# Kernel tuning notes

Measured on AMD Instinct MI355X. Metric: run time of the kernel, lower is better.

## Reference

```python
import jax, jax.numpy as jnp
import numpy as np

NEG = -1e30  # log-space -inf surrogate (safe for logaddexp in fp32)


def _ctc_mean_loss(y_true, y_pred):
    """tf.nn.ctc_loss with blank_index=-1, logit_length=T, label_length=#nonzero.

    y_true: [B, L] int labels, 0 = padding, packed at the front.
    y_pred: [B, T, C] logits. blank = C-1. Returns mean NLL over batch.
    """
    B, L = y_true.shape
    T, C = y_pred.shape[1], y_pred.shape[2]
    blank = C - 1
    S = 2 * L + 1  # extended label length (blanks interleaved)

    label_length = jnp.sum((y_true != 0).astype(jnp.int32), axis=1)  # [B]
    logp = jax.nn.log_softmax(y_pred, axis=-1)  # [B, T, C]

    # Extended sequence: blank, l1, blank, l2, ..., blank
    ext = jnp.full((B, S), blank, dtype=jnp.int32)
    ext = ext.at[:, 1::2].set(y_true.astype(jnp.int32))  # [B, S]

    # skip transition (s-2 -> s) allowed only at odd s>=3 when labels differ
    skip_ok = jnp.zeros((B, S), dtype=bool)
    skip_ok = skip_ok.at[:, 3::2].set(y_true[:, 1:] != y_true[:, :-1])

    # alpha_0
    alpha0 = jnp.full((B, S), NEG, dtype=logp.dtype)
    alpha0 = alpha0.at[:, 0].set(logp[:, 0, blank])
    alpha0 = alpha0.at[:, 1].set(
        jnp.take_along_axis(logp[:, 0, :], ext[:, 1:2], axis=1)[:, 0])

    def step(alpha, logp_t):  # alpha [B,S], logp_t [B,C]
        s1 = jnp.pad(alpha, ((0, 0), (1, 0)), constant_values=NEG)[:, :-1]
        s2 = jnp.pad(alpha, ((0, 0), (2, 0)), constant_values=NEG)[:, :-2]
        comb = jnp.logaddexp(jnp.logaddexp(alpha, s1),
                             jnp.where(skip_ok, s2, NEG))
        emit = jnp.take_along_axis(logp_t, ext, axis=1)  # [B,S]
        return comb + emit, None

    alphaT, _ = jax.lax.scan(step, alpha0, jnp.swapaxes(logp, 0, 1)[1:])

    # P(labels) = alpha_T[2l] + alpha_T[2l-1]  (last blank / last label)
    l = label_length
    idx = jnp.stack([2 * l, 2 * l - 1], axis=1)  # [B,2], l>=1 by construction
    fin = jnp.take_along_axis(alphaT, idx, axis=1)
    loss = -jnp.logaddexp(fin[:, 0], fin[:, 1])  # [B]
    return jnp.mean(loss)


def setup_inputs() -> dict:
    key = jax.random.key(0)
    k1, k2, k3 = jax.random.split(key, 3)
    B, T, L, C = 256, 512, 128, 128
    lengths = jax.random.randint(k1, (B,), L // 2, L + 1)  # labels per example
    vals = jax.random.randint(k2, (B, L), 1, C - 1)  # classes 1..C-2 (blank=C-1)
    mask = jnp.arange(L)[None, :] < lengths[:, None]
    y_true = jnp.where(mask, vals, 0).astype(jnp.int32)
    y_pred = jax.random.normal(k3, (B, T, C), dtype=jnp.float32)
    return {"y_true": y_true, "y_pred": y_pred}


def reference(y_true, y_pred):
    return _ctc_mean_loss(y_true, y_pred)
```

## Files before the change

kernel.cpp:

```cpp
#include <hip/hip_runtime.h>
#include <hip/hip_fp16.h>

#define LN2D 0.6931471805599453094172321

typedef float v2f __attribute__((ext_vector_type(2)));

__device__ __forceinline__ float shr1(float v, float fill) {
    return __int_as_float(__builtin_amdgcn_update_dpp(
        __float_as_int(fill), __float_as_int(v), 0x138 , 0xF, 0xF, false));
}
__device__ __forceinline__ float shl1(float v, float fill) {
    return __int_as_float(__builtin_amdgcn_update_dpp(
        __float_as_int(fill), __float_as_int(v), 0x130 , 0xF, 0xF, false));
}

__device__ __forceinline__ float wave_sum63(float x) {
    int t;
    t = __builtin_amdgcn_update_dpp(0, __float_as_int(x), 0x111, 0xF, 0xF, true);
    x += __int_as_float(t);
    t = __builtin_amdgcn_update_dpp(0, __float_as_int(x), 0x112, 0xF, 0xF, true);
    x += __int_as_float(t);
    t = __builtin_amdgcn_update_dpp(0, __float_as_int(x), 0x114, 0xF, 0xF, true);
    x += __int_as_float(t);
    t = __builtin_amdgcn_update_dpp(0, __float_as_int(x), 0x118, 0xF, 0xF, true);
    x += __int_as_float(t);
    t = __builtin_amdgcn_update_dpp(0, __float_as_int(x), 0x142, 0xA, 0xF, true);
    x += __int_as_float(t);
    t = __builtin_amdgcn_update_dpp(0, __float_as_int(x), 0x143, 0xC, 0xF, true);
    x += __int_as_float(t);
    return x;
}

__device__ __forceinline__ float wave_max63(float x) {
    int iv = __float_as_int(x); int t;
    t = __builtin_amdgcn_update_dpp(iv, iv, 0x111, 0xF, 0xF, false);
    x = fmaxf(x, __int_as_float(t)); iv = __float_as_int(x);
    t = __builtin_amdgcn_update_dpp(iv, iv, 0x112, 0xF, 0xF, false);
    x = fmaxf(x, __int_as_float(t)); iv = __float_as_int(x);
    t = __builtin_amdgcn_update_dpp(iv, iv, 0x114, 0xF, 0xF, false);
    x = fmaxf(x, __int_as_float(t)); iv = __float_as_int(x);
    t = __builtin_amdgcn_update_dpp(iv, iv, 0x118, 0xF, 0xF, false);
    x = fmaxf(x, __int_as_float(t)); iv = __float_as_int(x);
    t = __builtin_amdgcn_update_dpp(iv, iv, 0x142, 0xA, 0xF, false);
    x = fmaxf(x, __int_as_float(t)); iv = __float_as_int(x);
    t = __builtin_amdgcn_update_dpp(iv, iv, 0x143, 0xC, 0xF, false);
    x = fmaxf(x, __int_as_float(t));
    return x;
}

__device__ __forceinline__ float rdl63(float v) {
    return __int_as_float(__builtin_amdgcn_readlane(__float_as_int(v), 63));
}

#define VSTRIDE 260

__global__ __launch_bounds__(256) void ctc_half(const int* __restrict__ yt,
                                                const float* __restrict__ yp,
                                                float* __restrict__ V,
                                                int* __restrict__ E,
                                                float* __restrict__ accW) {
    constexpr int L = 128;
    const int bh   = blockIdx.x;
    const int b    = bh >> 1, h = bh & 1;
    const int w    = threadIdx.x >> 6;
    const int lane = threadIdx.x & 63;

    __shared__ int g[256][64];

    const int2 cc = *reinterpret_cast<const int2*>(yt + b * L + 2 * lane);
    const int c1 = cc.x, c3 = cc.y;
    const int sl1 = c1 >> 1, sh1v = (c1 & 1) << 4;
    const int sl3 = c3 >> 1, sh3v = (c3 & 1) << 4;

    float acc = 0.0f;
    const float* src = yp + ((size_t)b * 512 + h * 256 + w * 64) * 128 + lane * 2;
    v2f A8[8], B8[8];

#define ISSUE8(d_, p_)                                                         \
    asm volatile(                                                              \
        "global_load_dwordx2 %0, %8, off\n\t"                                  \
        "global_load_dwordx2 %1, %8, off offset:512\n\t"                       \
        "global_load_dwordx2 %2, %8, off offset:1024\n\t"                      \
        "global_load_dwordx2 %3, %8, off offset:1536\n\t"                      \
        "global_load_dwordx2 %4, %8, off offset:2048\n\t"                      \
        "global_load_dwordx2 %5, %8, off offset:2560\n\t"                      \
        "global_load_dwordx2 %6, %8, off offset:3072\n\t"                      \
        "global_load_dwordx2 %7, %8, off offset:3584"                          \
        : "=&v"(d_[0]), "=&v"(d_[1]), "=&v"(d_[2]), "=&v"(d_[3]),              \
          "=&v"(d_[4]), "=&v"(d_[5]), "=&v"(d_[6]), "=&v"(d_[7])               \
        : "v"(p_)                                                              \
        : "memory");

#define WAITN(n_)                                                              \
    {                                                                          \
        asm volatile("s_waitcnt vmcnt(" #n_ ")" ::: "memory");                 \
        __builtin_amdgcn_sched_barrier(0);                                     \
    }

#define PROC8(buf_, rb_)                                                       \
    {                                                                          \
        _Pragma("unroll")                                                      \
        for (int i = 0; i < 8; ++i) {                                          \
            const float vx = buf_[i].x, vy = buf_[i].y;                        \
            const float sall = rdl63(wave_sum63(__expf(vx) + __expf(vy)));     \
            const float xbv  = rdl63(vy);                \
            acc += __logf(sall) - xbv;                                         \
            const __half2 hh = __floats2half2_rn(vx, vy);                      \
            const int hb = __builtin_bit_cast(int, hh);                        \
            const int q1 = __shfl(hb, sl1, 64);                                \
            const int q3 = __shfl(hb, sl3, 64);                                \
            const float x1 = __half2float(__builtin_bit_cast(__half, (unsigned short)(q1 >> sh1v))); \
            const float x3 = __half2float(__builtin_bit_cast(__half, (unsigned short)(q3 >> sh3v))); \
            g[w * 64 + (rb_) + i][lane] =                                      \
                __builtin_bit_cast(int, __floats2half2_rn(x1 - xbv, x3 - xbv)); \
        }                                                                      \
    }

    ISSUE8(A8, src)
    ISSUE8(B8, src + 8 * 128)
    WAITN(8)  PROC8(A8, 0)   ISSUE8(A8, src + 16 * 128)
    WAITN(8)  PROC8(B8, 8)   ISSUE8(B8, src + 24 * 128)
    WAITN(8)  PROC8(A8, 16)  ISSUE8(A8, src + 32 * 128)
    WAITN(8)  PROC8(B8, 24)  ISSUE8(B8, src + 40 * 128)
    WAITN(8)  PROC8(A8, 32)  ISSUE8(A8, src + 48 * 128)
    WAITN(8)  PROC8(B8, 40)  ISSUE8(B8, src + 56 * 128)
    WAITN(8)  PROC8(A8, 48)
    WAITN(0)  PROC8(B8, 56)

    if (lane == 0) accW[bh * 4 + w] = acc;
    __syncthreads();

    if (w == 0) {
        const int cprev = __shfl_up(c3, 1, 64);
        const float sk1 = (lane > 0 && c1 != cprev) ? 1.0f : 0.0f;
        const float sk3 = (c3 != c1) ? 1.0f : 0.0f;
        const float skB3 = shl1(sk1, 0.0f);
        const int llen = __popcll(__ballot(c1 != 0)) + __popcll(__ballot(c3 != 0));

        float o0, o1, o2, o3, o4;
        int   Eacc = 0;

#define RENORM()                                                               \
    {                                                                          \
        float mr = fmaxf(fmaxf(fmaxf(o0, o1), fmaxf(o2, o3)), o4);             \
        const float mru = rdl63(wave_max63(mr));                               \
        const int ie = (__float_as_int(mru) >> 23) & 0xFF;                     \
        const float sc = __int_as_float((253 - ie) << 23);                     \
        o0 *= sc; o1 *= sc; o2 *= sc; o3 *= sc; o4 *= sc;                      \
        Eacc += ie - 126;                                                      \
    }

#define FSTEP(bits_, rn_)                                                      \
    {                                                                          \
        const float2 dd = __half22float2(__builtin_bit_cast(__half2, (bits_)));\
        const float e1 = __expf(dd.x);                                         \
        const float e3 = __expf(dd.y);                                         \
        const float pm = shr1(o3, 0.0f);                                       \
        const float n0 = o0 + pm;                                              \
        const float n1 = (o1 + o0 + sk1 * pm) * e1;                            \
        const float n2 = o2 + o1;                                              \
        const float n3 = (o3 + o2 + sk3 * o1) * e3;                            \
        o4 += o3;                                                              \
        o0 = n0; o1 = n1; o2 = n2; o3 = n3;                                    \
        if (rn_) RENORM();                                                     \
    }

#define BSTEP(bits_, rn_)                                                      \
    {                                                                          \
        const float2 dd = __half22float2(__builtin_bit_cast(__half2, (bits_)));\
        const float g1 = o1 * __expf(dd.x);                                    \
        const float g3 = o3 * __expf(dd.y);                                    \
        const float pm0 = shl1(o0, o4);          \
        const float pm1 = shl1(g1, 0.0f);        \
        const float n0 = o0 + g1;                                              \
        const float n1 = g1 + o2 + sk3 * g3;                                   \
        const float n2 = o2 + g3;                                              \
        const float n3 = g3 + pm0 + skB3 * pm1;                                \
        o0 = n0; o1 = n1; o2 = n2; o3 = n3;                                    \
        if (rn_) RENORM();                                                     \
    }

        if (h == 0) {
            {
                const float2 d0 = __half22float2(__builtin_bit_cast(__half2, g[0][lane]));
                o0 = (lane == 0) ? 1.0f : 0.0f;
                o1 = (lane == 0) ? __expf(d0.x) : 0.0f;
                o2 = 0.0f; o3 = 0.0f; o4 = 0.0f;
            }
            #pragma unroll
            for (int t = 1; t < 32; ++t) FSTEP(g[t][lane], false);
            for (int tb = 32; tb < 256; tb += 32) {
                #pragma unroll
                for (int j = 0; j < 32; ++j) FSTEP(g[tb + j][lane], (j == 0));
            }
        } else {
            const int sA = 2 * llen, sB = 2 * llen - 1;
            o0 = (4 * lane + 0 == sA) ? 1.0f : 0.0f;
            o1 = (4 * lane + 1 == sB) ? 1.0f : 0.0f;
            o2 = (4 * lane + 2 == sA) ? 1.0f : 0.0f;
            o3 = (4 * lane + 3 == sB) ? 1.0f : 0.0f;
            o4 = (llen == 128 && lane == 63) ? 1.0f : 0.0f;
            for (int sb = 0; sb < 256; sb += 32) {
                #pragma unroll
                for (int u = 1; u <= 32; ++u) BSTEP(g[256 - (sb + u)][lane], (u == 32));
            }
        }

        float* Vh = V + (size_t)bh * VSTRIDE;
        Vh[4 * lane + 0] = o0; Vh[4 * lane + 1] = o1;
        Vh[4 * lane + 2] = o2; Vh[4 * lane + 3] = o3;
        if (lane == 63) Vh[256] = o4;
        if (lane == 0)  E[bh] = Eacc;
#undef BSTEP
#undef FSTEP
#undef RENORM
    }
#undef PROC8
#undef WAITN
#undef ISSUE8
}

__global__ __launch_bounds__(64) void combine(const float* __restrict__ V,
                                              const int* __restrict__ E,
                                              const float* __restrict__ accW,
                                              float* __restrict__ loss) {
    const int b = blockIdx.x, lane = threadIdx.x;
    const float* Vf = V + (size_t)(2 * b) * VSTRIDE;
    const float* Vb = Vf + VSTRIDE;
    const float4 a = *reinterpret_cast<const float4*>(Vf + 4 * lane);
    const float4 c = *reinterpret_cast<const float4*>(Vb + 4 * lane);
    double p = (double)a.x * (double)c.x + (double)a.y * (double)c.y
             + (double)a.z * (double)c.z + (double)a.w * (double)c.w;
    if (lane == 63) p += (double)Vf[256] * (double)Vb[256];
    #pragma unroll
    for (int off = 32; off > 0; off >>= 1) p += __shfl_xor(p, off, 64);
    if (lane == 0) {
        float ls = 0.0f;
        #pragma unroll
        for (int j = 0; j < 8; ++j) ls += accW[8 * b + j];
        const double lg = log(p) + (double)(E[2 * b] + E[2 * b + 1]) * LN2D - (double)ls;
        loss[b] = -(float)lg;
    }
}

__global__ __launch_bounds__(256) void finalize(const float* __restrict__ loss,
                                                float* __restrict__ out) {
    __shared__ float red[256];
    const int tid = threadIdx.x;
    red[tid] = loss[tid];
    __syncthreads();
    for (int off = 128; off > 0; off >>= 1) {
        if (tid < off) red[tid] += red[tid + off];
        __syncthreads();
    }
    if (tid == 0) out[0] = red[0] * (1.0f / 256.0f);
}

extern "C" void kernel_launch(void* const* d_in, const int* in_sizes, int n_in,
                              void* d_out, int out_size, void* d_ws, size_t ws_size,
                              hipStream_t stream) {
    constexpr int B = 256;
    const int*   y_true = (const int*)d_in[0];
    const float* y_pred = (const float*)d_in[1];
    float* out = (float*)d_out;

    float* V    = (float*)d_ws;
    int*   E    = (int*)(V + 512 * VSTRIDE);
    float* accW = (float*)(E + 512);
    float* loss = accW + 2048;

    ctc_half<<<B * 2, 256, 0, stream>>>(y_true, y_pred, V, E, accW);
    combine<<<B, 64, 0, stream>>>(V, E, accW, loss);
    finalize<<<1, 256, 0, stream>>>(loss, out);
}
```

Baseline: 43.95 us.

## Store precomputed bf16 emission probabilities and prefetch LDS rows in recursion

```diff
diff --git a/kernel.cpp b/kernel.cpp
--- a/kernel.cpp
+++ b/kernel.cpp
@@ -50,6 +50,13 @@
 
 __device__ __forceinline__ float rdl63(float v) {
     return __int_as_float(__builtin_amdgcn_readlane(__float_as_int(v), 63));
+}
+
+__device__ __forceinline__ int pk_bf16(float a, float b) {
+    unsigned ua = __float_as_uint(a), ub = __float_as_uint(b);
+    ua = (ua + 0x7FFFu + ((ua >> 16) & 1u)) >> 16;
+    ub = (ub + 0x7FFFu + ((ub >> 16) & 1u)) & 0xFFFF0000u;
+    return (int)(ua | ub);
 }
 
 #define VSTRIDE 260
@@ -112,7 +119,7 @@
             const float x1 = __half2float(__builtin_bit_cast(__half, (unsigned short)(q1 >> sh1v))); \
             const float x3 = __half2float(__builtin_bit_cast(__half, (unsigned short)(q3 >> sh3v))); \
             g[w * 64 + (rb_) + i][lane] =                                      \
-                __builtin_bit_cast(int, __floats2half2_rn(x1 - xbv, x3 - xbv)); \
+                pk_bf16(__expf(x1 - xbv), __expf(x3 - xbv));                   \
         }                                                                      \
     }
 
@@ -139,6 +146,7 @@
 
         float o0, o1, o2, o3, o4;
         int   Eacc = 0;
+        int   er[8];
 
 #define RENORM()                                                               \
     {                                                                          \
@@ -152,9 +160,8 @@
 
 #define FSTEP(bits_, rn_)                                                      \
     {                                                                          \
-        const float2 dd = __half22float2(__builtin_bit_cast(__half2, (bits_)));\
-        const float e1 = __expf(dd.x);                                         \
-        const float e3 = __expf(dd.y);                                         \
+        const float e1 = __int_as_float((bits_) << 16);                        \
+        const float e3 = __int_as_float((bits_) & 0xFFFF0000);                 \
         const float pm = shr1(o3, 0.0f);                                       \
         const float n0 = o0 + pm;                                              \
         const float n1 = (o1 + o0 + sk1 * pm) * e1;                            \
@@ -167,9 +174,10 @@
 
 #define BSTEP(bits_, rn_)                                                      \
     {                                                                          \
-        const float2 dd = __half22float2(__builtin_bit_cast(__half2, (bits_)));\
-        const float g1 = o1 * __expf(dd.x);                                    \
-        const float g3 = o3 * __expf(dd.y);                                    \
+        const float e1 = __int_as_float((bits_) << 16);                        \
+        const float e3 = __int_as_float((bits_) & 0xFFFF0000);                 \
+        const float g1 = o1 * e1;                                              \
+        const float g3 = o3 * e3;                                              \
         const float pm0 = shl1(o0, o4);          \
         const float pm1 = shl1(g1, 0.0f);        \
         const float n0 = o0 + g1;                                              \
@@ -181,29 +189,47 @@
     }
 
         if (h == 0) {
+            #pragma unroll
+            for (int i = 0; i < 8; ++i) er[i] = g[i][lane];
             {
-                const float2 d0 = __half22float2(__builtin_bit_cast(__half2, g[0][lane]));
+                const float e10 = __int_as_float(er[0] << 16);
                 o0 = (lane == 0) ? 1.0f : 0.0f;
-                o1 = (lane == 0) ? __expf(d0.x) : 0.0f;
+                o1 = (lane == 0) ? e10 : 0.0f;
                 o2 = 0.0f; o3 = 0.0f; o4 = 0.0f;
             }
-            #pragma unroll
-            for (int t = 1; t < 32; ++t) FSTEP(g[t][lane], false);
-            for (int tb = 32; tb < 256; tb += 32) {
+            er[0] = g[8][lane];
+            #pragma unroll
+            for (int t = 1; t < 8; ++t) { FSTEP(er[t], false); er[t] = g[t + 8][lane]; }
+            #pragma unroll
+            for (int tb = 8; tb < 248; tb += 8) {
                 #pragma unroll
-                for (int j = 0; j < 32; ++j) FSTEP(g[tb + j][lane], (j == 0));
+                for (int j = 0; j < 8; ++j) {
+                    FSTEP(er[j], ((tb + j) & 31) == 0);
+                    er[j] = g[tb + j + 8][lane];
+                }
             }
+            #pragma unroll
+            for (int t = 248; t < 256; ++t) FSTEP(er[t & 7], false);
         } else {
+            #pragma unroll
+            for (int i = 0; i < 8; ++i) er[i] = g[255 - i][lane];
             const int sA = 2 * llen, sB = 2 * llen - 1;
             o0 = (4 * lane + 0 == sA) ? 1.0f : 0.0f;
             o1 = (4 * lane + 1 == sB) ? 1.0f : 0.0f;
             o2 = (4 * lane + 2 == sA) ? 1.0f : 0.0f;
             o3 = (4 * lane + 3 == sB) ? 1.0f : 0.0f;
             o4 = (llen == 128 && lane == 63) ? 1.0f : 0.0f;
-            for (int sb = 0; sb < 256; sb += 32) {
+            #pragma unroll
+            for (int kb = 0; kb < 248; kb += 8) {
                 #pragma unroll
-                for (int u = 1; u <= 32; ++u) BSTEP(g[256 - (sb + u)][lane], (u == 32));
+                for (int j = 0; j < 8; ++j) {
+                    const int r = 255 - (kb + j);
+                    BSTEP(er[j], (r & 31) == 0);
+                    er[j] = g[r - 8][lane];
+                }
             }
+            #pragma unroll
+            for (int k = 248; k < 256; ++k) BSTEP(er[k & 7], ((255 - k) & 31) == 0);
         }
 
         float* Vh = V + (size_t)bh * VSTRIDE;
```

Result: faster. 40.80 us (median of 2 runs) (-7.2%).

## Fuse forward/backward CTC halves into one block with interleaved recursions and fp8 emissions

Applied to the files above, without the earlier changes.

```diff
diff --git a/kernel.cpp b/kernel.cpp
--- a/kernel.cpp
+++ b/kernel.cpp
@@ -52,20 +52,30 @@
     return __int_as_float(__builtin_amdgcn_readlane(__float_as_int(v), 63));
 }
 
-#define VSTRIDE 260
-
-__global__ __launch_bounds__(256) void ctc_half(const int* __restrict__ yt,
-                                                const float* __restrict__ yp,
-                                                float* __restrict__ V,
-                                                int* __restrict__ E,
-                                                float* __restrict__ accW) {
+__device__ __forceinline__ unsigned short pk_fp8(float a, float b) {
+    const unsigned short ha = __builtin_bit_cast(unsigned short, __float2half_rn(a));
+    const unsigned short hb = __builtin_bit_cast(unsigned short, __float2half_rn(b));
+    const unsigned ua = ((unsigned)ha + 0x80u) >> 8;
+    const unsigned ub = (((unsigned)hb + 0x80u) >> 8) << 8;
+    return (unsigned short)(ua | ub);
+}
+__device__ __forceinline__ float dec_lo(unsigned short u) {
+    return __half2float(__builtin_bit_cast(__half, (unsigned short)((u & 0xFFu) << 8)));
+}
+__device__ __forceinline__ float dec_hi(unsigned short u) {
+    return __half2float(__builtin_bit_cast(__half, (unsigned short)(u & 0xFF00u)));
+}
+
+__global__ __launch_bounds__(512) void ctc_fused(const int* __restrict__ yt,
+                                                 const float* __restrict__ yp,
+                                                 float* __restrict__ part,
+                                                 float* __restrict__ accW) {
     constexpr int L = 128;
-    const int bh   = blockIdx.x;
-    const int b    = bh >> 1, h = bh & 1;
+    const int b    = blockIdx.x;
     const int w    = threadIdx.x >> 6;
     const int lane = threadIdx.x & 63;
 
-    __shared__ int g[256][64];
+    __shared__ unsigned short g[512][64];
 
     const int2 cc = *reinterpret_cast<const int2*>(yt + b * L + 2 * lane);
     const int c1 = cc.x, c3 = cc.y;
@@ -73,7 +83,7 @@
     const int sl3 = c3 >> 1, sh3v = (c3 & 1) << 4;
 
     float acc = 0.0f;
-    const float* src = yp + ((size_t)b * 512 + h * 256 + w * 64) * 128 + lane * 2;
+    const float* src = yp + ((size_t)b * 512 + w * 64) * 128 + lane * 2;
     v2f A8[8], B8[8];
 
 #define ISSUE8(d_, p_)                                                         \
@@ -111,8 +121,7 @@
             const int q3 = __shfl(hb, sl3, 64);                                \
             const float x1 = __half2float(__builtin_bit_cast(__half, (unsigned short)(q1 >> sh1v))); \
             const float x3 = __half2float(__builtin_bit_cast(__half, (unsigned short)(q3 >> sh3v))); \
-            g[w * 64 + (rb_) + i][lane] =                                      \
-                __builtin_bit_cast(int, __floats2half2_rn(x1 - xbv, x3 - xbv)); \
+            g[w * 64 + (rb_) + i][lane] = pk_fp8(__expf(x1 - xbv), __expf(x3 - xbv)); \
         }                                                                      \
     }
 
@@ -127,7 +136,7 @@
     WAITN(8)  PROC8(A8, 48)
     WAITN(0)  PROC8(B8, 56)
 
-    if (lane == 0) accW[bh * 4 + w] = acc;
+    if (lane == 0) accW[b * 8 + w] = acc;
     __syncthreads();
 
     if (w == 0) {
@@ -138,23 +147,24 @@
         const int llen = __popcll(__ballot(c1 != 0)) + __popcll(__ballot(c3 != 0));
 
         float o0, o1, o2, o3, o4;
-        int   Eacc = 0;
-
-#define RENORM()                                                               \
-    {                                                                          \
-        float mr = fmaxf(fmaxf(fmaxf(o0, o1), fmaxf(o2, o3)), o4);             \
+        float q0, q1, q2, q3, q4;
+        int   EF = 0, EB = 0;
+        unsigned short fr[8], br[8];
+
+#define RENORM5(a0_, a1_, a2_, a3_, a4_, Ec_)                                  \
+    {                                                                          \
+        float mr = fmaxf(fmaxf(fmaxf(a0_, a1_), fmaxf(a2_, a3_)), a4_);        \
         const float mru = rdl63(wave_max63(mr));                               \
         const int ie = (__float_as_int(mru) >> 23) & 0xFF;                     \
         const float sc = __int_as_float((253 - ie) << 23);                     \
-        o0 *= sc; o1 *= sc; o2 *= sc; o3 *= sc; o4 *= sc;                      \
-        Eacc += ie - 126;                                                      \
+        a0_ *= sc; a1_ *= sc; a2_ *= sc; a3_ *= sc; a4_ *= sc;                 \
+        Ec_ += ie - 126;                                                       \
     }
 
 #define FSTEP(bits_, rn_)                                                      \
     {                                                                          \
-        const float2 dd = __half22float2(__builtin_bit_cast(__half2, (bits_)));\
-        const float e1 = __expf(dd.x);                                         \
-        const float e3 = __expf(dd.y);                                         \
+        const float e1 = dec_lo(bits_);                                        \
+        const float e3 = dec_hi(bits_);                                        \
         const float pm = shr1(o3, 0.0f);                                       \
         const float n0 = o0 + pm;                                              \
         const float n1 = (o1 + o0 + sk1 * pm) * e1;                            \
@@ -162,92 +172,91 @@
         const float n3 = (o3 + o2 + sk3 * o1) * e3;                            \
         o4 += o3;                                                              \
         o0 = n0; o1 = n1; o2 = n2; o3 = n3;                                    \
-        if (rn_) RENORM();                                                     \
+        if (rn_) RENORM5(o0, o1, o2, o3, o4, EF);                              \
     }
 
 #define BSTEP(bits_, rn_)                                                      \
     {                                                                          \
-        const float2 dd = __half22float2(__builtin_bit_cast(__half2, (bits_)));\
-        const float g1 = o1 * __expf(dd.x);                                    \
-        const float g3 = o3 * __expf(dd.y);                                    \
-        const float pm0 = shl1(o0, o4);          \
+        const float e1 = dec_lo(bits_);                                        \
+        const float e3 = dec_hi(bits_);                                        \
+        const float g1 = q1 * e1;                                              \
+        const float g3 = q3 * e3;                                              \
+        const float pm0 = shl1(q0, q4);          \
         const float pm1 = shl1(g1, 0.0f);        \
-        const float n0 = o0 + g1;                                              \
-        const float n1 = g1 + o2 + sk3 * g3;                                   \
-        const float n2 = o2 + g3;                                              \
+        const float n0 = q0 + g1;                                              \
+        const float n1 = g1 + q2 + sk3 * g3;                                   \
+        const float n2 = q2 + g3;                                              \
         const float n3 = g3 + pm0 + skB3 * pm1;                                \
-        o0 = n0; o1 = n1; o2 = n2; o3 = n3;                                    \
-        if (rn_) RENORM();                                                     \
-    }
-
-        if (h == 0) {
-            {
-                const float2 d0 = __half22float2(__builtin_bit_cast(__half2, g[0][lane]));
-                o0 = (lane == 0) ? 1.0f : 0.0f;
-                o1 = (lane == 0) ? __expf(d0.x) : 0.0f;
-                o2 = 0.0f; o3 = 0.0f; o4 = 0.0f;
+        q0 = n0; q1 = n1; q2 = n2; q3 = n3;                                    \
+        if (rn_) RENORM5(q0, q1, q2, q3, q4, EB);                              \
+    }
+
+        #pragma unroll
+        for (int i = 0; i < 8; ++i) { fr[i] = g[i][lane]; br[i] = g[511 - i][lane]; }
+
+        {
+            const float e10 = dec_lo(fr[0]);
+            o0 = (lane == 0) ? 1.0f : 0.0f;
+            o1 = (lane == 0) ? e10 : 0.0f;
+            o2 = 0.0f; o3 = 0.0f; o4 = 0.0f;
+        }
+        {
+            const int sA = 2 * llen, sB = 2 * llen - 1;
+            q0 = (4 * lane + 0 == sA) ? 1.0f : 0.0f;
+            q1 = (4 * lane + 1 == sB) ? 1.0f : 0.0f;
+            q2 = (4 * lane + 2 == sA) ? 1.0f : 0.0f;
+            q3 = (4 * lane + 3 == sB) ? 1.0f : 0.0f;
+            q4 = (llen == 128 && lane == 63) ? 1.0f : 0.0f;
+        }
+
+        BSTEP(br[0], false);
+        fr[0] = g[8][lane]; br[0] = g[503][lane];
+        #pragma unroll
+        for (int k = 1; k < 8; ++k) {
+            FSTEP(fr[k], false);
+            BSTEP(br[k], false);
+            fr[k] = g[k + 8][lane]; br[k] = g[511 - k - 8][lane];
+        }
+        for (int kb = 8; kb < 248; kb += 8) {
+            #pragma unroll
+            for (int j = 0; j < 8; ++j) {
+                const int k = kb + j;
+                FSTEP(fr[j], (k & 31) == 0);
+                BSTEP(br[j], (k & 31) == 31);
+                fr[j] = g[k + 8][lane]; br[j] = g[511 - k - 8][lane];
             }
-            #pragma unroll
-            for (int t = 1; t < 32; ++t) FSTEP(g[t][lane], false);
-            for (int tb = 32; tb < 256; tb += 32) {
-                #pragma unroll
-                for (int j = 0; j < 32; ++j) FSTEP(g[tb + j][lane], (j == 0));
-            }
-        } else {
-            const int sA = 2 * llen, sB = 2 * llen - 1;
-            o0 = (4 * lane + 0 == sA) ? 1.0f : 0.0f;
-            o1 = (4 * lane + 1 == sB) ? 1.0f : 0.0f;
-            o2 = (4 * lane + 2 == sA) ? 1.0f : 0.0f;
-            o3 = (4 * lane + 3 == sB) ? 1.0f : 0.0f;
-            o4 = (llen == 128 && lane == 63) ? 1.0f : 0.0f;
-            for (int sb = 0; sb < 256; sb += 32) {
-                #pragma unroll
-                for (int u = 1; u <= 32; ++u) BSTEP(g[256 - (sb + u)][lane], (u == 32));
-            }
-        }
-
-        float* Vh = V + (size_t)bh * VSTRIDE;
-        Vh[4 * lane + 0] = o0; Vh[4 * lane + 1] = o1;
-        Vh[4 * lane + 2] = o2; Vh[4 * lane + 3] = o3;
-        if (lane == 63) Vh[256] = o4;
-        if (lane == 0)  E[bh] = Eacc;
+        }
+        #pragma unroll
+        for (int k = 248; k < 256; ++k) {
+            FSTEP(fr[k & 7], false);
+            BSTEP(br[k & 7], (k & 31) == 31);
+        }
+
+        double p = (double)o0 * (double)q0 + (double)o1 * (double)q1
+                 + (double)o2 * (double)q2 + (double)o3 * (double)q3;
+        if (lane == 63) p += (double)o4 * (double)q4;
+        #pragma unroll
+        for (int off = 32; off > 0; off >>= 1) p += __shfl_xor(p, off, 64);
+        if (lane == 0)
+            part[b] = (float)(log(p) + (double)(EF + EB) * LN2D);
 #undef BSTEP
 #undef FSTEP
-#undef RENORM
+#undef RENORM5
     }
 #undef PROC8
 #undef WAITN
 #undef ISSUE8
 }
 
-__global__ __launch_bounds__(64) void combine(const float* __restrict__ V,
-                                              const int* __restrict__ E,
-                                              const float* __restrict__ accW,
-                                              float* __restrict__ loss) {
-    const int b = blockIdx.x, lane = threadIdx.x;
-    const float* Vf = V + (size_t)(2 * b) * VSTRIDE;
-    const float* Vb = Vf + VSTRIDE;
-    const float4 a = *reinterpret_cast<const float4*>(Vf + 4 * lane);
-    const float4 c = *reinterpret_cast<const float4*>(Vb + 4 * lane);
-    double p = (double)a.x * (double)c.x + (double)a.y * (double)c.y
-             + (double)a.z * (double)c.z + (double)a.w * (double)c.w;
-    if (lane == 63) p += (double)Vf[256] * (double)Vb[256];
-    #pragma unroll
-    for (int off = 32; off > 0; off >>= 1) p += __shfl_xor(p, off, 64);
-    if (lane == 0) {
-        float ls = 0.0f;
-        #pragma unroll
-        for (int j = 0; j < 8; ++j) ls += accW[8 * b + j];
-        const double lg = log(p) + (double)(E[2 * b] + E[2 * b + 1]) * LN2D - (double)ls;
-        loss[b] = -(float)lg;
-    }
-}
-
-__global__ __launch_bounds__(256) void finalize(const float* __restrict__ loss,
+__global__ __launch_bounds__(256) void finalize(const float* __restrict__ part,
+                                                const float* __restrict__ accW,
                                                 float* __restrict__ out) {
     __shared__ float red[256];
     const int tid = threadIdx.x;
-    red[tid] = loss[tid];
+    float ls = 0.0f;
+    #pragma unroll
+    for (int j = 0; j < 8; ++j) ls += accW[tid * 8 + j];
+    red[tid] = -(part[tid] - ls);
     __syncthreads();
     for (int off = 128; off > 0; off >>= 1) {
         if (tid < off) red[tid] += red[tid + off];
@@ -264,12 +273,9 @@
     const float* y_pred = (const float*)d_in[1];
     float* out = (float*)d_out;
 
-    float* V    = (float*)d_ws;
-    int*   E    = (int*)(V + 512 * VSTRIDE);
-    float* accW = (float*)(E + 512);
-    float* loss = accW + 2048;
-
-    ctc_half<<<B * 2, 256, 0, stream>>>(y_true, y_pred, V, E, accW);
-    combine<<<B, 64, 0, stream>>>(V, E, accW, loss);
-    finalize<<<1, 256, 0, stream>>>(loss, out);
-}
+    float* part = (float*)d_ws;
+    float* accW = part + B;
+
+    ctc_fused<<<B, 512, 0, stream>>>(y_true, y_pred, part, accW);
+    finalize<<<1, 256, 0, stream>>>(part, accW, out);
+}
```

Measured after the change: 45.24 us. 2.9% more time.
